# Kernel tuning notes

Hardware: AMD Instinct MI355X
Metric: run time of the kernel (lower is better)

Reference implementation:

```python
import jax, jax.numpy as jnp
import numpy as np

N_NODES = 50000
N_EDGES = 800000
IN_F = 128
OUT_F = 32
HEADS = 4
EDGE_DIM = 8
ALPHA = 0.2  # LeakyReLU negative slope


def setup_inputs() -> dict:
    key = jax.random.key(0)
    k0, k1, k2, k3, k4 = jax.random.split(key, 5)
    x = jax.random.normal(k0, (N_NODES, IN_F), dtype=jnp.float32)
    edge_index = jax.random.randint(k1, (2, N_EDGES), 0, N_NODES, dtype=jnp.int32)
    edge_attr = jax.random.normal(k2, (N_EDGES, EDGE_DIM), dtype=jnp.float32)
    # xavier-ish init for parameters
    W = jax.random.normal(k3, (HEADS, IN_F, OUT_F), dtype=jnp.float32) * (1.0 / np.float32(np.sqrt(IN_F)))
    a = jax.random.normal(k4, (HEADS, 2 * OUT_F + EDGE_DIM, 1), dtype=jnp.float32) * np.float32(0.1)
    return {"x": x, "edge_index": edge_index, "edge_attr": edge_attr, "W": W, "a": a}


def reference(x, edge_index, edge_attr, W, a):
    n_nodes = x.shape[0]
    out_f = W.shape[2]
    src, dst = edge_index[0], edge_index[1]

    # per-head linear transform: (N, H, O)
    xt = jnp.einsum('ni,hio->nho', x, W)
    x_src = xt[src]  # (E, H, O) edge gather
    x_dst = xt[dst]  # (E, H, O)

    # split attention vector a = [a_src | a_dst | a_edge]; equivalent to
    # einsum('ehi,hio->eho', cat([x_src, x_dst, edge]), a) without the concat
    av = a[..., 0]                      # (H, 2O+D)
    a_s = av[:, :out_f]                 # (H, O)
    a_d = av[:, out_f:2 * out_f]        # (H, O)
    a_e = av[:, 2 * out_f:]             # (H, D)
    e = (jnp.einsum('eho,ho->eh', x_src, a_s)
         + jnp.einsum('eho,ho->eh', x_dst, a_d)
         + edge_attr @ a_e.T)           # (E, H)
    e = jnp.where(e > 0, e, ALPHA * e)  # LeakyReLU

    # segment (per-destination) softmax over incoming edges, per head
    max_e = jax.ops.segment_max(e, dst, num_segments=n_nodes)   # (N, H), -inf on empty
    max_e = jnp.where(jnp.isneginf(max_e), jnp.zeros_like(max_e), max_e)
    exp_e = jnp.exp(e - max_e[dst])                             # (E, H)
    sum_exp = jax.ops.segment_sum(exp_e, dst, num_segments=n_nodes)  # (N, H)
    attention = exp_e / (sum_exp[dst] + 1e-10)                  # (E, H)

    # weighted scatter-add aggregation
    weighted = x_src * attention[:, :, None]                    # (E, H, O)
    out = jax.ops.segment_sum(weighted, dst, num_segments=n_nodes)  # (N, H, O)
    return out.reshape(n_nodes, -1)  # concat=True -> (N, H*O)
```

## Files before the change

kernel.cpp:

```cpp
#include <hip/hip_runtime.h>
#include <hip/hip_fp16.h>

#define N_NODES 50000
#define N_EDGES 800000
#define IN_F    128
#define OUT_F   32
#define HEADS   4
#define EDGE_DIM 8
#define LRELU_ALPHA 0.2f

#define EPB 2048
#define BT  1024
#define EPT (EPB / BT)
#define NBUCK 98
#define NBLK_A ((N_EDGES + EPB - 1) / EPB)
#define NODES_PER_BUCK 512
#define CAP 10240

typedef float    floatx4 __attribute__((ext_vector_type(4)));
typedef unsigned uintx4  __attribute__((ext_vector_type(4)));
typedef short    short4v __attribute__((ext_vector_type(4)));
typedef short    short8v __attribute__((ext_vector_type(8)));
typedef float    f32x4   __attribute__((ext_vector_type(4)));

__device__ __forceinline__ unsigned f2bf(float f) {
  unsigned u = __float_as_uint(f);
  return (u + 0x7fffu + ((u >> 16) & 1u)) >> 16;
}

__global__ __launch_bounds__(256) void k_transform(
    const float* __restrict__ x, const float* __restrict__ W,
    unsigned* __restrict__ xtb) {
  __shared__ short sxb[64][136];
  __shared__ short wt[128][136];
  const int t = threadIdx.x;
  const int n0 = blockIdx.x * 64;

#pragma unroll
  for (int r = 0; r < 64; ++r) {
    const int idx = r * 256 + t;
    const int h = idx >> 12;
    const int i = (idx >> 5) & 127;
    const int o = idx & 31;
    wt[h * 32 + o][i] = (short)f2bf(W[idx]);
  }

#pragma unroll
  for (int r = 0; r < 8; ++r) {
    const int f = r * 256 + t;
    const int node = f >> 5;
    const int i4 = (f & 31) * 4;
    const int n = n0 + node;
    float4 v = make_float4(0.f, 0.f, 0.f, 0.f);
    if (n < N_NODES) v = *reinterpret_cast<const float4*>(&x[(size_t)n * 128 + i4]);
    short4v s4;
    s4.x = (short)f2bf(v.x);
    s4.y = (short)f2bf(v.y);
    s4.z = (short)f2bf(v.z);
    s4.w = (short)f2bf(v.w);
    *reinterpret_cast<short4v*>(&sxb[node][i4]) = s4;
  }
  __syncthreads();

  const int w = t >> 6;
  const int lane = t & 63;
  const int r16 = lane & 15;
  const int kg = lane >> 4;

  f32x4 acc[8];
#pragma unroll
  for (int nt = 0; nt < 8; ++nt) acc[nt] = (f32x4)(0.f);

#pragma unroll
  for (int kk = 0; kk < 4; ++kk) {
    const short8v afrag =
        *reinterpret_cast<const short8v*>(&sxb[w * 16 + r16][kk * 32 + kg * 8]);
#pragma unroll
    for (int nt = 0; nt < 8; ++nt) {
      const short8v bfrag =
          *reinterpret_cast<const short8v*>(&wt[nt * 16 + r16][kk * 32 + kg * 8]);
      acc[nt] = __builtin_amdgcn_mfma_f32_16x16x32_bf16(afrag, bfrag, acc[nt],
                                                        0, 0, 0);
    }
  }

#pragma unroll
  for (int nt = 0; nt < 8; ++nt) {
#pragma unroll
    for (int reg = 0; reg < 4; ++reg) {
      const float v = acc[nt][reg];
      const float vp = __shfl_xor(v, 1, 64);
      if (!(lane & 1)) {
        const int node = n0 + w * 16 + kg * 4 + reg;
        if (node < N_NODES) {
          const unsigned u = f2bf(v) | (f2bf(vp) << 16);
          xtb[(size_t)node * 64 + nt * 8 + (r16 >> 1)] = u;
        }
      }
    }
  }
}

__global__ __launch_bounds__(256) void k_alpha(
    const unsigned* __restrict__ xtb, const float* __restrict__ a,
    float* __restrict__ alpha_src, float* __restrict__ alpha_dst,
    unsigned* __restrict__ bfill) {
  const int t = threadIdx.x;
  if (blockIdx.x == 0 && t < NBUCK) bfill[t] = (unsigned)(t * CAP);

  const int node = blockIdx.x * 64 + (t >> 2);
  if (node >= N_NODES) return;
  const int q = t & 3;
  const unsigned* __restrict__ row = &xtb[(size_t)node * 64 + q * 16];
  const float* __restrict__ as = &a[q * 72];
  const float* __restrict__ ad = &a[q * 72 + 32];
  float s = 0.f, d = 0.f;
#pragma unroll
  for (int j = 0; j < 16; ++j) {
    const unsigned u = row[j];
    const float lo = __uint_as_float(u << 16);
    const float hi = __uint_as_float(u & 0xffff0000u);
    s = fmaf(lo, as[2 * j], s);
    s = fmaf(hi, as[2 * j + 1], s);
    d = fmaf(lo, ad[2 * j], d);
    d = fmaf(hi, ad[2 * j + 1], d);
  }
  alpha_src[node * 4 + q] = s;
  alpha_dst[node * 4 + q] = d;
}

__device__ __forceinline__ uintx4 make_entry(
    int e, int src, int dst, const float* __restrict__ ea,
    const float* __restrict__ a, const float* __restrict__ alpha_src,
    const float* __restrict__ alpha_dst) {
  const floatx4 ev0 = __builtin_nontemporal_load(
      reinterpret_cast<const floatx4*>(&ea[(size_t)e * EDGE_DIM]));
  const floatx4 ev1 = __builtin_nontemporal_load(
      reinterpret_cast<const floatx4*>(&ea[(size_t)e * EDGE_DIM + 4]));
  const float4 als = *reinterpret_cast<const float4*>(&alpha_src[src * 4]);
  const float4 ald = *reinterpret_cast<const float4*>(&alpha_dst[dst * 4]);
  const float* alsp = reinterpret_cast<const float*>(&als);
  const float* aldp = reinterpret_cast<const float*>(&ald);
  unsigned sh[4];
#pragma unroll
  for (int h = 0; h < HEADS; ++h) {
    float s = alsp[h] + aldp[h];
    const float* ae = &a[h * 72 + 64];
    s = fmaf(ev0.x, ae[0], s);
    s = fmaf(ev0.y, ae[1], s);
    s = fmaf(ev0.z, ae[2], s);
    s = fmaf(ev0.w, ae[3], s);
    s = fmaf(ev1.x, ae[4], s);
    s = fmaf(ev1.y, ae[5], s);
    s = fmaf(ev1.z, ae[6], s);
    s = fmaf(ev1.w, ae[7], s);
    s = s > 0.f ? s : LRELU_ALPHA * s;
    sh[h] = (unsigned)__half_as_ushort(__float2half(s));
  }
  uintx4 ent;
  ent.x = (unsigned)src;
  ent.y = sh[0] | (sh[1] << 16);
  ent.z = sh[2] | (sh[3] << 16);
  ent.w = (unsigned)dst;
  return ent;
}

__global__ __launch_bounds__(BT) void k_binsort(
    const int* __restrict__ ei, const float* __restrict__ ea,
    const float* __restrict__ a, const float* __restrict__ alpha_src,
    const float* __restrict__ alpha_dst, unsigned* __restrict__ bfill,
    uintx4* __restrict__ stage) {
  __shared__ uintx4 sent[EPB];
  __shared__ unsigned short sbk[EPB];
  __shared__ unsigned lhist[128];
  __shared__ unsigned lscan[128];
  __shared__ unsigned gb[128];
  const int t = threadIdx.x;
  const int e0 = blockIdx.x * EPB;
  const int nvalid = min(EPB, N_EDGES - e0);

  if (t < 128) lhist[t] = 0u;
  __syncthreads();

  uintx4 ent[EPT];
  int bk[EPT];
  int lpos[EPT];
#pragma unroll
  for (int k = 0; k < EPT; ++k) {
    const int e = e0 + k * BT + t;
    bk[k] = -1;
    if (e < N_EDGES) {
      const int src = __builtin_nontemporal_load(&ei[e]);
      const int dst = __builtin_nontemporal_load(&ei[N_EDGES + e]);
      ent[k] = make_entry(e, src, dst, ea, a, alpha_src, alpha_dst);
      bk[k] = dst >> 9;
      lpos[k] = (int)atomicAdd(&lhist[bk[k]], 1u);
    }
  }
  __syncthreads();

  if (t < 128) lscan[t] = lhist[t];
  __syncthreads();
#pragma unroll
  for (int off = 1; off < 128; off <<= 1) {
    unsigned v = 0u;
    if (t < 128 && t >= off) v = lscan[t - off];
    __syncthreads();
    if (t < 128) lscan[t] += v;
    __syncthreads();
  }
  if (t < NBUCK) {
    const unsigned cnt = lhist[t];
    lscan[t] -= cnt;
    gb[t] = cnt ? atomicAdd(&bfill[t], cnt) : 0u;
  }
  __syncthreads();

#pragma unroll
  for (int k = 0; k < EPT; ++k) {
    if (bk[k] >= 0) {
      const int p = (int)lscan[bk[k]] + lpos[k];
      sent[p] = ent[k];
      sbk[p] = (unsigned short)bk[k];
    }
  }
  __syncthreads();

#pragma unroll
  for (int k = 0; k < EPT; ++k) {
    const int p = k * BT + t;
    if (p < nvalid) {
      const int b = sbk[p];
      stage[gb[b] + (unsigned)(p - (int)lscan[b])] = sent[p];
    }
  }
}

__global__ __launch_bounds__(128) void k_scan_s(
    const unsigned* __restrict__ bfill, unsigned* __restrict__ bstart) {
  __shared__ unsigned s[128];
  const int t = threadIdx.x;
  const unsigned cnt = (t < NBUCK) ? (bfill[t] - (unsigned)(t * CAP)) : 0u;
  s[t] = cnt;
  __syncthreads();
#pragma unroll
  for (int off = 1; off < 128; off <<= 1) {
    unsigned v = (t >= off) ? s[t - off] : 0u;
    __syncthreads();
    s[t] += v;
    __syncthreads();
  }
  if (t < NBUCK) bstart[t] = s[t] - cnt;
  if (t == 0) bstart[NBUCK] = N_EDGES;
}

__global__ __launch_bounds__(1024) void k_place(
    const unsigned* __restrict__ bfill, const unsigned* __restrict__ bstart,
    const uintx4* __restrict__ stage, unsigned* __restrict__ rs,
    uintx4* __restrict__ csr) {
  __shared__ unsigned lbuf[NODES_PER_BUCK];
  __shared__ unsigned wsum[8];
  const int b = blockIdx.x;
  const int t = threadIdx.x;
  const int node0 = b << 9;
  const int nn = min(NODES_PER_BUCK, N_NODES - node0);
  const unsigned base = (unsigned)(b * CAP);
  const unsigned cnt = bfill[b] - base;
  const unsigned bs = bstart[b];

  if (t < NODES_PER_BUCK) lbuf[t] = 0u;
  __syncthreads();

  for (unsigned i = t; i < cnt; i += 1024) {
    const unsigned dst = __builtin_nontemporal_load(&stage[base + i]).w;
    atomicAdd(&lbuf[dst - (unsigned)node0], 1u);
  }
  __syncthreads();

  const unsigned c = (t < NODES_PER_BUCK) ? lbuf[t] : 0u;
  unsigned incl = c;
  const int lane = t & 63;
#pragma unroll
  for (int off = 1; off < 64; off <<= 1) {
    const unsigned n = __shfl_up(incl, off, 64);
    if (lane >= off) incl += n;
  }
  if (t < NODES_PER_BUCK && lane == 63) wsum[t >> 6] = incl;
  __syncthreads();
  if (t < 8) {
    const unsigned wv = wsum[t];
    unsigned wincl = wv;
#pragma unroll
    for (int off = 1; off < 8; off <<= 1) {
      const unsigned n = __shfl_up(wincl, off, 64);
      if (t >= off) wincl += n;
    }
    wsum[t] = wincl - wv;
  }
  __syncthreads();
  if (t < NODES_PER_BUCK) {
    const unsigned excl = incl - c + wsum[t >> 6];
    lbuf[t] = bs + excl;
    if (t < nn) rs[node0 + t] = bs + excl;
  }
  if (b == NBUCK - 1 && t == 0) rs[N_NODES] = N_EDGES;
  __syncthreads();

  for (unsigned i = t; i < cnt; i += 1024) {
    const uintx4 ent = __builtin_nontemporal_load(&stage[base + i]);
    const unsigned slot = atomicAdd(&lbuf[ent.w - (unsigned)node0], 1u);
    csr[slot] = ent;
  }
}

__device__ __forceinline__ float ent_score(const uintx4& ent, int hA) {
  const unsigned uu = (hA < 2) ? ent.y : ent.z;
  const unsigned us = (hA & 1) ? (uu >> 16) : (uu & 0xffffu);
  return __half2float(__ushort_as_half((unsigned short)us));
}

__global__ __launch_bounds__(256) void k_agg(
    const unsigned* __restrict__ rs, const uintx4* __restrict__ csr,
    const unsigned* __restrict__ xtb, float* __restrict__ out) {
  const int lane = threadIdx.x & 63;
  const int dst = (int)((blockIdx.x * (unsigned)blockDim.x + threadIdx.x) >> 6);
  if (dst >= N_NODES) return;

  const unsigned j0 = rs[dst];
  const unsigned j1 = rs[dst + 1];
  const int deg = (int)(j1 - j0);

  float a0 = 0.f, a1 = 0.f, lsum = 0.f;

  if (deg > 0) {
    const int rounds = (deg + 15) >> 4;
    const int sub = lane >> 2;
    const int hA = lane & 3;
    const int hB = lane >> 4;

    for (int r = 0; r < rounds; ++r) {
      const int base = (int)j0 + r * 16;
      const int j = base + sub;
      uintx4 ent;
      if (j < (int)j1) {
        ent = __builtin_nontemporal_load(&csr[j]);
      } else {
        ent.x = 0u; ent.y = 0xfc00fc00u; ent.z = 0xfc00fc00u; ent.w = 0u;
      }
      const float w = __expf(ent_score(ent, hA));
      lsum += w;
      const int sx = (int)ent.x;
#pragma unroll
      for (int jj = 0; jj < 16; ++jj) {
        const int src = __shfl(sx, 4 * jj, 64);
        const float wj = __shfl(w, 4 * jj + hB, 64);
        const unsigned u = xtb[(size_t)src * 64 + lane];
        a0 = fmaf(wj, __uint_as_float(u << 16), a0);
        a1 = fmaf(wj, __uint_as_float(u & 0xffff0000u), a1);
      }
    }
    lsum += __shfl_xor(lsum, 4, 64);
    lsum += __shfl_xor(lsum, 8, 64);
    lsum += __shfl_xor(lsum, 16, 64);
    lsum += __shfl_xor(lsum, 32, 64);
    lsum = __shfl(lsum, hB, 64);
  }

  const float inv = 1.0f / (lsum + 1e-10f);
  out[(size_t)dst * 128 + lane * 2 + 0] = a0 * inv;
  out[(size_t)dst * 128 + lane * 2 + 1] = a1 * inv;
}

extern "C" void kernel_launch(void* const* d_in, const int* in_sizes, int n_in,
                              void* d_out, int out_size, void* d_ws,
                              size_t ws_size, hipStream_t stream) {
  const float* x = (const float*)d_in[0];
  const int* ei = (const int*)d_in[1];
  const float* ea = (const float*)d_in[2];
  const float* W = (const float*)d_in[3];
  const float* a = (const float*)d_in[4];
  float* out = (float*)d_out;

  char* p = (char*)d_ws;
  unsigned* xtb = (unsigned*)p;     p += (size_t)N_NODES * 64 * 4;
  uintx4* csr = (uintx4*)p;         p += (size_t)N_EDGES * 16;
  uintx4* stage = (uintx4*)p;       p += (size_t)NBUCK * CAP * 16;
  float* alpha_src = (float*)p;     p += (size_t)N_NODES * 4 * 4;
  float* alpha_dst = (float*)p;     p += (size_t)N_NODES * 4 * 4;
  unsigned* rs = (unsigned*)p;      p += (size_t)(N_NODES + 1) * 4;
  unsigned* bfill = (unsigned*)p;   p += 128 * 4;
  unsigned* bstart = (unsigned*)p;  p += 128 * 4;

  k_transform<<<(N_NODES + 63) / 64, 256, 0, stream>>>(x, W, xtb);
  k_alpha<<<(N_NODES + 63) / 64, 256, 0, stream>>>(xtb, a, alpha_src,
                                                   alpha_dst, bfill);
  k_binsort<<<NBLK_A, BT, 0, stream>>>(ei, ea, a, alpha_src, alpha_dst, bfill,
                                       stage);
  k_scan_s<<<1, 128, 0, stream>>>(bfill, bstart);
  k_place<<<NBUCK, 1024, 0, stream>>>(bfill, bstart, stage, rs, csr);
  k_agg<<<(N_NODES * 64 + 255) / 256, 256, 0, stream>>>(rs, csr, xtb, out);
}
```

Baseline: 114.0 us.

## Fuse alpha into transform, fold bucket scan into place, unroll aggregation loop

Computes the per-node attention projections directly from the MFMA accumulators inside the transform kernel, so the separate alpha kernel and its re-read of the bf16 features go away. The bucket prefix scan is recomputed redundantly in every k_place block, which removes the single-block scan kernel and one launch. The aggregation loop now handles two 16-edge rounds per iteration to expose more independent loads, and the output uses nontemporal stores. Alpha values now come from fp32 accumulators instead of bf16-rounded features, so they differ slightly, and the two-round loop raises register pressure.

Measured after the change: 113.8 us. No clear change (-0.1%).

```diff
diff --git a/kernel.cpp b/kernel.cpp
--- a/kernel.cpp
+++ b/kernel.cpp
@@ -30,11 +30,15 @@
 
 __global__ __launch_bounds__(256) void k_transform(
     const float* __restrict__ x, const float* __restrict__ W,
-    unsigned* __restrict__ xtb) {
+    const float* __restrict__ a, unsigned* __restrict__ xtb,
+    float* __restrict__ alpha_src, float* __restrict__ alpha_dst,
+    unsigned* __restrict__ bfill) {
   __shared__ short sxb[64][136];
   __shared__ short wt[128][136];
   const int t = threadIdx.x;
   const int n0 = blockIdx.x * 64;
+
+  if (blockIdx.x == 0 && t < NBUCK) bfill[t] = (unsigned)(t * CAP);
 
 #pragma unroll
   for (int r = 0; r < 64; ++r) {
@@ -99,34 +103,36 @@
       }
     }
   }
-}
-
-__global__ __launch_bounds__(256) void k_alpha(
-    const unsigned* __restrict__ xtb, const float* __restrict__ a,
-    float* __restrict__ alpha_src, float* __restrict__ alpha_dst,
-    unsigned* __restrict__ bfill) {
-  const int t = threadIdx.x;
-  if (blockIdx.x == 0 && t < NBUCK) bfill[t] = (unsigned)(t * CAP);
-
-  const int node = blockIdx.x * 64 + (t >> 2);
-  if (node >= N_NODES) return;
-  const int q = t & 3;
-  const unsigned* __restrict__ row = &xtb[(size_t)node * 64 + q * 16];
-  const float* __restrict__ as = &a[q * 72];
-  const float* __restrict__ ad = &a[q * 72 + 32];
-  float s = 0.f, d = 0.f;
-#pragma unroll
-  for (int j = 0; j < 16; ++j) {
-    const unsigned u = row[j];
-    const float lo = __uint_as_float(u << 16);
-    const float hi = __uint_as_float(u & 0xffff0000u);
-    s = fmaf(lo, as[2 * j], s);
-    s = fmaf(hi, as[2 * j + 1], s);
-    d = fmaf(lo, ad[2 * j], d);
-    d = fmaf(hi, ad[2 * j + 1], d);
-  }
-  alpha_src[node * 4 + q] = s;
-  alpha_dst[node * 4 + q] = d;
+
+  float asv[8], adv[8];
+#pragma unroll
+  for (int nt = 0; nt < 8; ++nt) {
+    const int h = nt >> 1;
+    const int o = (nt & 1) * 16 + r16;
+    asv[nt] = a[h * 72 + o];
+    adv[nt] = a[h * 72 + 32 + o];
+  }
+#pragma unroll
+  for (int reg = 0; reg < 4; ++reg) {
+    const int node = n0 + w * 16 + kg * 4 + reg;
+    float s[4], d[4];
+#pragma unroll
+    for (int h = 0; h < 4; ++h) {
+      s[h] = acc[2 * h][reg] * asv[2 * h] + acc[2 * h + 1][reg] * asv[2 * h + 1];
+      d[h] = acc[2 * h][reg] * adv[2 * h] + acc[2 * h + 1][reg] * adv[2 * h + 1];
+#pragma unroll
+      for (int off = 1; off < 16; off <<= 1) {
+        s[h] += __shfl_xor(s[h], off, 64);
+        d[h] += __shfl_xor(d[h], off, 64);
+      }
+    }
+    if (r16 < 4 && node < N_NODES) {
+      const float sv = (r16 == 0) ? s[0] : (r16 == 1) ? s[1] : (r16 == 2) ? s[2] : s[3];
+      const float dv = (r16 == 0) ? d[0] : (r16 == 1) ? d[1] : (r16 == 2) ? d[2] : d[3];
+      alpha_src[node * 4 + r16] = sv;
+      alpha_dst[node * 4 + r16] = dv;
+    }
+  }
 }
 
 __device__ __forceinline__ uintx4 make_entry(
@@ -236,37 +242,36 @@
   }
 }
 
-__global__ __launch_bounds__(128) void k_scan_s(
-    const unsigned* __restrict__ bfill, unsigned* __restrict__ bstart) {
-  __shared__ unsigned s[128];
-  const int t = threadIdx.x;
-  const unsigned cnt = (t < NBUCK) ? (bfill[t] - (unsigned)(t * CAP)) : 0u;
-  s[t] = cnt;
-  __syncthreads();
-#pragma unroll
-  for (int off = 1; off < 128; off <<= 1) {
-    unsigned v = (t >= off) ? s[t - off] : 0u;
-    __syncthreads();
-    s[t] += v;
-    __syncthreads();
-  }
-  if (t < NBUCK) bstart[t] = s[t] - cnt;
-  if (t == 0) bstart[NBUCK] = N_EDGES;
-}
-
 __global__ __launch_bounds__(1024) void k_place(
-    const unsigned* __restrict__ bfill, const unsigned* __restrict__ bstart,
-    const uintx4* __restrict__ stage, unsigned* __restrict__ rs,
-    uintx4* __restrict__ csr) {
+    const unsigned* __restrict__ bfill, const uintx4* __restrict__ stage,
+    unsigned* __restrict__ rs, uintx4* __restrict__ csr) {
   __shared__ unsigned lbuf[NODES_PER_BUCK];
   __shared__ unsigned wsum[8];
+  __shared__ unsigned bscan[128];
   const int b = blockIdx.x;
   const int t = threadIdx.x;
   const int node0 = b << 9;
   const int nn = min(NODES_PER_BUCK, N_NODES - node0);
   const unsigned base = (unsigned)(b * CAP);
+
+  unsigned myc = 0u;
+  if (t < 128) {
+    myc = (t < NBUCK) ? (bfill[t] - (unsigned)(t * CAP)) : 0u;
+    bscan[t] = myc;
+  }
+  __syncthreads();
+#pragma unroll
+  for (int off = 1; off < 128; off <<= 1) {
+    unsigned v = 0u;
+    if (t < 128 && t >= off) v = bscan[t - off];
+    __syncthreads();
+    if (t < 128) bscan[t] += v;
+    __syncthreads();
+  }
+  if (t < 128 && t == b) bscan[127] = bscan[t] - myc;
+  __syncthreads();
   const unsigned cnt = bfill[b] - base;
-  const unsigned bs = bstart[b];
+  const unsigned bs = (b == 0) ? 0u : bscan[b - 1];
 
   if (t < NODES_PER_BUCK) lbuf[t] = 0u;
   __syncthreads();
@@ -338,25 +343,42 @@
     const int hA = lane & 3;
     const int hB = lane >> 4;
 
-    for (int r = 0; r < rounds; ++r) {
-      const int base = (int)j0 + r * 16;
-      const int j = base + sub;
-      uintx4 ent;
-      if (j < (int)j1) {
-        ent = __builtin_nontemporal_load(&csr[j]);
-      } else {
-        ent.x = 0u; ent.y = 0xfc00fc00u; ent.z = 0xfc00fc00u; ent.w = 0u;
+    const uintx4 pad = {0u, 0xfc00fc00u, 0xfc00fc00u, 0u};
+
+    for (int r = 0; r < rounds; r += 2) {
+      const int base0 = (int)j0 + r * 16;
+      const int jA = base0 + sub;
+      const int jB = base0 + 16 + sub;
+      const bool has1 = (r + 1) < rounds;
+      const uintx4 entA = (jA < (int)j1) ? __builtin_nontemporal_load(&csr[jA]) : pad;
+      const uintx4 entB =
+          (has1 && jB < (int)j1) ? __builtin_nontemporal_load(&csr[jB]) : pad;
+
+      {
+        const float w = __expf(ent_score(entA, hA));
+        lsum += w;
+        const int sx = (int)entA.x;
+#pragma unroll
+        for (int jj = 0; jj < 16; ++jj) {
+          const int src = __shfl(sx, 4 * jj, 64);
+          const float wj = __shfl(w, 4 * jj + hB, 64);
+          const unsigned u = xtb[(size_t)src * 64 + lane];
+          a0 = fmaf(wj, __uint_as_float(u << 16), a0);
+          a1 = fmaf(wj, __uint_as_float(u & 0xffff0000u), a1);
+        }
       }
-      const float w = __expf(ent_score(ent, hA));
-      lsum += w;
-      const int sx = (int)ent.x;
-#pragma unroll
-      for (int jj = 0; jj < 16; ++jj) {
-        const int src = __shfl(sx, 4 * jj, 64);
-        const float wj = __shfl(w, 4 * jj + hB, 64);
-        const unsigned u = xtb[(size_t)src * 64 + lane];
-        a0 = fmaf(wj, __uint_as_float(u << 16), a0);
-        a1 = fmaf(wj, __uint_as_float(u & 0xffff0000u), a1);
+      if (has1) {
+        const float w = __expf(ent_score(entB, hA));
+        lsum += w;
+        const int sx = (int)entB.x;
+#pragma unroll
+        for (int jj = 0; jj < 16; ++jj) {
+          const int src = __shfl(sx, 4 * jj, 64);
+          const float wj = __shfl(w, 4 * jj + hB, 64);
+          const unsigned u = xtb[(size_t)src * 64 + lane];
+          a0 = fmaf(wj, __uint_as_float(u << 16), a0);
+          a1 = fmaf(wj, __uint_as_float(u & 0xffff0000u), a1);
+        }
       }
     }
     lsum += __shfl_xor(lsum, 4, 64);
@@ -367,8 +389,11 @@
   }
 
   const float inv = 1.0f / (lsum + 1e-10f);
-  out[(size_t)dst * 128 + lane * 2 + 0] = a0 * inv;
-  out[(size_t)dst * 128 + lane * 2 + 1] = a1 * inv;
+  floatx4 o;
+  o.x = a0 * inv;
+  o.y = a1 * inv;
+  __builtin_nontemporal_store(o.x, &out[(size_t)dst * 128 + lane * 2 + 0]);
+  __builtin_nontemporal_store(o.y, &out[(size_t)dst * 128 + lane * 2 + 1]);
 }
 
 extern "C" void kernel_launch(void* const* d_in, const int* in_sizes, int n_in,
@@ -389,14 +414,11 @@
   float* alpha_dst = (float*)p;     p += (size_t)N_NODES * 4 * 4;
   unsigned* rs = (unsigned*)p;      p += (size_t)(N_NODES + 1) * 4;
   unsigned* bfill = (unsigned*)p;   p += 128 * 4;
-  unsigned* bstart = (unsigned*)p;  p += 128 * 4;
-
-  k_transform<<<(N_NODES + 63) / 64, 256, 0, stream>>>(x, W, xtb);
-  k_alpha<<<(N_NODES + 63) / 64, 256, 0, stream>>>(xtb, a, alpha_src,
-                                                   alpha_dst, bfill);
+
+  k_transform<<<(N_NODES + 63) / 64, 256, 0, stream>>>(x, W, a, xtb, alpha_src,
+                                                       alpha_dst, bfill);
   k_binsort<<<NBLK_A, BT, 0, stream>>>(ei, ea, a, alpha_src, alpha_dst, bfill,
                                        stage);
-  k_scan_s<<<1, 128, 0, stream>>>(bfill, bstart);
-  k_place<<<NBUCK, 1024, 0, stream>>>(bfill, bstart, stage, rs, csr);
+  k_place<<<NBUCK, 1024, 0, stream>>>(bfill, stage, rs, csr);
   k_agg<<<(N_NODES * 64 + 255) / 256, 256, 0, stream>>>(rs, csr, xtb, out);
 }
```
